# Kernel tuning notes

Hardware: AMD Instinct MI355X
Metric: run time of the kernel (lower is better)

Reference implementation:

```python
import jax, jax.numpy as jnp
import numpy as np

DG = 8   # deformable groups
K = 9    # 3x3 kernel taps


def _conv3x3(x, w, b):
    y = jax.lax.conv_general_dilated(x, w, (1, 1), ((1, 1), (1, 1)),
                                     dimension_numbers=('NCHW', 'OIHW', 'NCHW'))
    return y + b[None, :, None, None]


def _deform_conv_v2(x, off_y, off_x, mask, w, b):
    # x: [B,C,H,W], off_*/mask: [B,DG,K,H,W], w: [Cout,C,3,3], b: [Cout]
    B, C, H, W = x.shape
    cpg = C // DG
    k = jnp.arange(K)
    ky = (k // 3 - 1).astype(x.dtype)[None, None, :, None, None]
    kx = (k % 3 - 1).astype(x.dtype)[None, None, :, None, None]
    hh = jnp.arange(H, dtype=x.dtype)[None, None, None, :, None]
    ww = jnp.arange(W, dtype=x.dtype)[None, None, None, None, :]
    py = hh + ky + off_y            # sampling rows  [B,DG,K,H,W]
    px = ww + kx + off_x            # sampling cols
    y0 = jnp.floor(py); x0 = jnp.floor(px)
    ly = py - y0; lx = px - x0
    xf = x.reshape(B, DG, cpg, H * W)

    def corner(yi, xi):
        valid = ((yi >= 0) & (yi < H) & (xi >= 0) & (xi < W)).astype(x.dtype)
        idx = (jnp.clip(yi, 0, H - 1) * W + jnp.clip(xi, 0, W - 1)).astype(jnp.int32)
        idxb = jnp.broadcast_to(idx.reshape(B, DG, 1, K * H * W), (B, DG, cpg, K * H * W))
        v = jnp.take_along_axis(xf, idxb, axis=3).reshape(B, DG, cpg, K, H, W)
        return v, valid

    v00, m00 = corner(y0, x0)
    v01, m01 = corner(y0, x0 + 1)
    v10, m10 = corner(y0 + 1, x0)
    v11, m11 = corner(y0 + 1, x0 + 1)
    w00 = ((1 - ly) * (1 - lx) * m00)[:, :, None]
    w01 = ((1 - ly) * lx * m01)[:, :, None]
    w10 = (ly * (1 - lx) * m10)[:, :, None]
    w11 = (ly * lx * m11)[:, :, None]
    val = (v00 * w00 + v01 * w01 + v10 * w10 + v11 * w11) * mask[:, :, None]
    wr = w.reshape(w.shape[0], DG, cpg, K)
    return jnp.einsum('bgckhw,ogck->bohw', val, wr) + b[None, :, None, None]


def reference(feat_l, feat_s, w_atten, w_fsm, w_off, w_cm, b_cm, w_dcn, b_dcn):
    B, C, H, W = feat_l.shape
    # bilinear upsample (align_corners=False == half-pixel centers, matches jax.image.resize)
    feat_up = jax.image.resize(feat_s, (B, feat_s.shape[1], H, W), method='bilinear')
    # FeatureSelectionModule: SE-style gate + residual + 1x1 proj
    gap = feat_l.mean(axis=(2, 3))                       # [B,C]
    atten = jax.nn.sigmoid(gap @ w_atten.T)[:, :, None, None]
    xg = feat_l * (1.0 + atten)                          # x + x*atten
    feat_arm = jnp.einsum('bchw,oc->bohw', xg, w_fsm)
    # offset feature: 1x1 conv over cat([feat_arm, 2*feat_up])
    cat = jnp.concatenate([feat_arm, feat_up * 2.0], axis=1)
    off_feat = jnp.einsum('bchw,oc->bohw', cat, w_off)
    # dcn_v2 internal conv_offset_mask -> o1, o2, mask
    om = _conv3x3(off_feat, w_cm, b_cm)                  # [B, DG*3*K, H, W]
    n = DG * K
    off_y = om[:, :n].reshape(B, DG, K, H, W)
    off_x = om[:, n:2 * n].reshape(B, DG, K, H, W)
    mask = jax.nn.sigmoid(om[:, 2 * n:]).reshape(B, DG, K, H, W)
    out = _deform_conv_v2(feat_up, off_y, off_x, mask, w_dcn, b_dcn)
    return jax.nn.relu(out) + feat_arm


def setup_inputs() -> dict:
    key = jax.random.key(0)
    ks = jax.random.split(key, 9)
    B, C, H, W = 8, 128, 64, 64
    return {
        'feat_l': jax.random.normal(ks[0], (B, C, H, W), jnp.float32),
        'feat_s': jax.random.normal(ks[1], (B, C, H // 2, W // 2), jnp.float32),
        'w_atten': jax.random.normal(ks[2], (C, C), jnp.float32) / np.sqrt(C),
        'w_fsm': jax.random.normal(ks[3], (C, C), jnp.float32) / np.sqrt(C),
        'w_off': jax.random.normal(ks[4], (C, 2 * C), jnp.float32) / np.sqrt(2 * C),
        'w_cm': jax.random.normal(ks[5], (DG * 3 * K, C, 3, 3), jnp.float32) * 0.01,
        'b_cm': jnp.zeros((DG * 3 * K,), jnp.float32),
        'w_dcn': jax.random.normal(ks[6], (C, C, 3, 3), jnp.float32) / np.sqrt(C * 9),
        'b_dcn': jax.random.normal(ks[7], (C,), jnp.float32) * 0.01,
    }
```

## Files before the change

kernel.cpp:

```cpp
#include <hip/hip_runtime.h>
#include <hip/hip_bf16.h>

constexpr int Bn = 8, Cn = 128, Hn = 64, Wn = 64, HWn = Hn * Wn;
constexpr int DGn = 8, Kn = 9, CMn = 216;
constexpr int Hs = 32, Ws = 32, HWs = Hs * Ws;

typedef __attribute__((ext_vector_type(8))) short bf16x8;
typedef __attribute__((ext_vector_type(4))) float f32x4;

constexpr long OFF_FLAG = 0;
constexpr long OFF_FLB  = 256;
constexpr long OFF_FUPB = OFF_FLB  + (long)Bn*HWn*Cn/2;
constexpr long OFF_OFT  = OFF_FUPB + (long)Bn*HWn*Cn/2;
constexpr long OFF_WCT  = OFF_OFT  + (long)Bn*HWn*Cn/2;
constexpr long OFF_WDT  = OFF_WCT  + (long)18*224*64/2 + 64;
constexpr long OFF_P    = OFF_WDT  + (long)Kn*Cn*Cn/2 + 64;
constexpr long OFF_W1TB = OFF_P    + 16384;
constexpr long OFF_WCAT = OFF_W1TB + (long)Bn*Cn*Cn/2;
constexpr long OFF_BCM  = OFF_WCAT + (long)Bn*Cn*256/2;
constexpr long OFF_BDC  = OFF_BCM + 256;
constexpr long OFF_GAP  = OFF_BDC + 256;
constexpr long OFF_AT   = OFF_GAP + 1024;
constexpr long OFF_FARM = OFF_AT  + 1024;
constexpr long OFF_OM   = OFF_FARM + (long)Bn*Cn*HWn;

static __device__ __forceinline__ float ldin(const void* p, long i, bool isbf) {
  if (isbf) return __bfloat162float(((const __hip_bfloat16*)p)[i]);
  return ((const float*)p)[i];
}
static __device__ __forceinline__ unsigned short f2b(float f) {
  unsigned u = __builtin_bit_cast(unsigned, f);
  u += 0x7FFFu + ((u >> 16) & 1u);
  return (unsigned short)(u >> 16);
}
static __device__ __forceinline__ unsigned pack2(float v0, float v1) {
  return ((unsigned)f2b(v1) << 16) | (unsigned)f2b(v0);
}
static __device__ __forceinline__ float b2f(unsigned short s) {
  return __builtin_bit_cast(float, ((unsigned)s) << 16);
}

#define GLOAD_LDS16(g, l) __builtin_amdgcn_global_load_lds( \
    (const __attribute__((address_space(1))) void*)(g),     \
    (__attribute__((address_space(3))) void*)(l), 16, 0, 0)

__global__ __launch_bounds__(256) void k_detect(const unsigned int* __restrict__ p,
                                                int* __restrict__ flag,
                                                float* __restrict__ gap) {
  __shared__ int cnt[256];
  int t = threadIdx.x;
  int c = 0;
  for (int i = 0; i < 4; ++i) {
    unsigned v = p[t * 4 + i];
    unsigned e = (v >> 7) & 0xFFu;
    c += (e >= 118u && e <= 130u) ? 1 : 0;
  }
  cnt[t] = c;
#pragma unroll
  for (int i = 0; i < 4; ++i) gap[t + i * 256] = 0.f;
  __syncthreads();
  for (int s = 128; s > 0; s >>= 1) {
    if (t < s) cnt[t] += cnt[t + s];
    __syncthreads();
  }
  if (t == 0) *flag = (cnt[0] > 512) ? 1 : 0;
}

__global__ __launch_bounds__(256) void k_prep(const void* __restrict__ b_cm,
                                              const void* __restrict__ b_dcn,
                                              const void* __restrict__ w_cm,
                                              const void* __restrict__ w_dcn,
                                              const void* __restrict__ woff,
                                              const void* __restrict__ wfsm,
                                              float* __restrict__ bcm_d,
                                              float* __restrict__ bdc_d,
                                              unsigned short* __restrict__ wcb,
                                              unsigned short* __restrict__ wdb,
                                              float* __restrict__ P,
                                              const int* __restrict__ flag) {
  const int bid = blockIdx.x, t = threadIdx.x;
  const bool isbf = (*flag != 0);
  if (bid == 0) {
    if (t < CMn) bcm_d[t] = ldin(b_cm, t, isbf);
    if (t < Cn)  bdc_d[t] = ldin(b_dcn, t, isbf);
    return;
  }
  if (bid < 1 + 1008) {
    int i = (bid - 1) * 256 + t;
    if (i >= 18 * 224 * 64) return;
    int s = i / (224 * 64);
    int rem = i % (224 * 64);
    int oc = rem >> 6, c_off = rem & 63;
    int tap = s >> 1, ck = s & 1;
    int c = ck * 64 + c_off;
    float v = 0.f;
    if (oc < CMn) v = ldin(w_cm, ((long)oc * Cn + c) * Kn + tap, isbf);
    int chunk = c_off >> 3, e = c_off & 7;
    int pc = chunk ^ (oc & 7);
    wcb[(long)s * 14336 + oc * 64 + pc * 8 + e] = f2b(v);
    return;
  }
  if (bid < 1 + 1008 + 576) {
    int i = (bid - 1 - 1008) * 256 + t;
    if (i >= Kn * Cn * Cn) return;
    int e = i & 7, lh = (i >> 3) & 3, o = (i >> 5) & 127;
    int ks = (i >> 12) & 3, k = i >> 14;
    int c = ks * 32 + lh * 8 + e;
    wdb[i] = f2b(ldin(w_dcn, ((long)o * Cn + c) * Kn + k, isbf));
    return;
  }
  {
    int idx = (bid - 1 - 1008 - 576) * 256 + t;
    if (idx >= Cn * Cn) return;
    int o = idx >> 7, k = idx & 127;
    float s = 0.f;
    for (int c = 0; c < Cn; ++c)
      s += ldin(woff, (long)o * 256 + c, isbf) * ldin(wfsm, (long)c * Cn + k, isbf);
    P[idx] = s;
  }
}

__global__ __launch_bounds__(256) void k_cvtlup(const void* __restrict__ feat_l,
                                                const void* __restrict__ fs,
                                                unsigned short* __restrict__ flb,
                                                unsigned short* __restrict__ fupb,
                                                float* __restrict__ gap,
                                                const int* __restrict__ flag) {
  __shared__ float sh[8448];
  const int b = blockIdx.y, t = threadIdx.x;
  const bool isbf = (*flag != 0);
  if (blockIdx.z == 0) {
    const int p0 = blockIdx.x * 64;
    for (int i = t; i < 8192; i += 256) {
      int c = i >> 6, p = i & 63;
      sh[c * 65 + p] = ldin(feat_l, (long)(b * Cn + c) * HWn + p0 + p, isbf);
    }
    __syncthreads();
    if (t < 128) {
      float s = 0.f;
#pragma unroll
      for (int p = 0; p < 64; ++p) s += sh[t * 65 + p];
      atomicAdd(&gap[b * Cn + t], s * (1.0f / HWn));
    }
    for (int i = t; i < 1024; i += 256) {
      int p = i >> 4, ch = (i & 15) * 8;
      uint4 pk;
      pk.x = pack2(sh[(ch + 0) * 65 + p], sh[(ch + 1) * 65 + p]);
      pk.y = pack2(sh[(ch + 2) * 65 + p], sh[(ch + 3) * 65 + p]);
      pk.z = pack2(sh[(ch + 4) * 65 + p], sh[(ch + 5) * 65 + p]);
      pk.w = pack2(sh[(ch + 6) * 65 + p], sh[(ch + 7) * 65 + p]);
      *(uint4*)(flb + (((long)(b * HWn + p0 + p)) << 7) + ch) = pk;
    }
  } else {
    const int h = blockIdx.x;
    int iy0; float fy;
    if (h & 1) { iy0 = (h - 1) >> 1; fy = 0.25f; } else { iy0 = (h >> 1) - 1; fy = 0.75f; }
    int iy1 = min(iy0 + 1, Hs - 1); iy0 = max(iy0, 0);
    for (int i = t; i < 8192; i += 256) {
      int sel = i >> 12, c = (i >> 5) & 127, x = i & 31;
      int iy = sel ? iy1 : iy0;
      sh[sel * 4224 + c * 33 + x] = ldin(fs, (long)(b * Cn + c) * HWs + iy * Ws + x, isbf);
    }
    __syncthreads();
    for (int i = t; i < 1024; i += 256) {
      int w = i >> 4, ch0 = (i & 15) * 8;
      int ix0; float fx;
      if (w & 1) { ix0 = (w - 1) >> 1; fx = 0.25f; } else { ix0 = (w >> 1) - 1; fx = 0.75f; }
      int ix1 = min(ix0 + 1, Ws - 1); ix0 = max(ix0, 0);
      float v[8];
#pragma unroll
      for (int j = 0; j < 8; ++j) {
        int c = ch0 + j;
        v[j] = (1.f - fy) * ((1.f - fx) * sh[c * 33 + ix0] + fx * sh[c * 33 + ix1]) +
               fy         * ((1.f - fx) * sh[4224 + c * 33 + ix0] + fx * sh[4224 + c * 33 + ix1]);
      }
      uint4 pk;
      pk.x = pack2(v[0], v[1]); pk.y = pack2(v[2], v[3]);
      pk.z = pack2(v[4], v[5]); pk.w = pack2(v[6], v[7]);
      *(uint4*)(fupb + (((long)(b * HWn + h * Wn + w)) << 7) + ch0) = pk;
    }
  }
}

__global__ __launch_bounds__(256) void k_atten(const float* __restrict__ gap,
                                               const void* __restrict__ wat,
                                               float* __restrict__ at1p,
                                               const int* __restrict__ flag) {
  int tid = blockIdx.x * 256 + threadIdx.x;
  if (tid >= Bn * Cn) return;
  int b = tid >> 7, o = tid & 127;
  bool isbf = (*flag != 0);
  const float* g = gap + b * Cn;
  float s = 0.f;
  for (int c = 0; c < Cn; ++c) s += g[c] * ldin(wat, (long)o * Cn + c, isbf);
  at1p[tid] = 1.0f + 1.0f / (1.0f + expf(-s));
}

__global__ __launch_bounds__(256) void k_wprep(const void* __restrict__ wfsm,
                                               const void* __restrict__ woff,
                                               const float* __restrict__ P,
                                               const float* __restrict__ at1p,
                                               unsigned short* __restrict__ w1tb,
                                               unsigned short* __restrict__ wcat,
                                               const int* __restrict__ flag) {
  int idx = blockIdx.x * 256 + threadIdx.x;
  if (idx >= Bn * 49152) return;
  bool isbf = (*flag != 0);
  int b = idx / 49152, r = idx % 49152;
  if (r < 16384) {
    int o = r >> 7, k = r & 127;
    w1tb[((long)(b * Cn + o) << 7) + k] =
        f2b(ldin(wfsm, (long)o * Cn + k, isbf) * at1p[b * Cn + k]);
  } else {
    r -= 16384;
    int o = r >> 8, k = r & 255;
    float v = (k < 128) ? P[o * Cn + k] * at1p[b * Cn + k]
                        : 2.0f * ldin(woff, (long)o * 256 + k, isbf);
    wcat[((long)(b * Cn + o) << 8) + k] = f2b(v);
  }
}

__global__ __launch_bounds__(256) void k_fao(const unsigned short* __restrict__ flb,
                                             const unsigned short* __restrict__ fupb,
                                             const unsigned short* __restrict__ w1tb,
                                             const unsigned short* __restrict__ wcat,
                                             unsigned short* __restrict__ farm,
                                             unsigned short* __restrict__ oftb) {
  const int b = blockIdx.y, m0 = blockIdx.x * 32;
  const int t = threadIdx.x, lane = t & 63, wv = t >> 6;
  const int lm = lane & 15, lh = lane >> 4;
  f32x4 accF[2][2], accO[2][2];
#pragma unroll
  for (int mt = 0; mt < 2; ++mt)
#pragma unroll
    for (int nt = 0; nt < 2; ++nt) {
      accF[mt][nt] = (f32x4){0.f, 0.f, 0.f, 0.f};
      accO[mt][nt] = (f32x4){0.f, 0.f, 0.f, 0.f};
    }
  const unsigned short* A0 = flb + ((long)b << 19);
  const unsigned short* A1 = fupb + ((long)b << 19);
  const unsigned short* BwF = w1tb + ((long)b << 14);
  const unsigned short* BwO = wcat + ((long)b << 15);
#pragma unroll
  for (int ks = 0; ks < 4; ++ks) {
    int c0 = ks * 32 + lh * 8;
    bf16x8 bfvF[2], bfvO[2];
#pragma unroll
    for (int nt = 0; nt < 2; ++nt) {
      int o = wv * 32 + nt * 16 + lm;
      bfvF[nt] = *(const bf16x8*)(BwF + ((long)o << 7) + c0);
      bfvO[nt] = *(const bf16x8*)(BwO + ((long)o << 8) + c0);
    }
#pragma unroll
    for (int mt = 0; mt < 2; ++mt) {
      bf16x8 af = *(const bf16x8*)(A0 + (((long)(m0 + mt * 16 + lm)) << 7) + c0);
#pragma unroll
      for (int nt = 0; nt < 2; ++nt) {
        accF[mt][nt] = __builtin_amdgcn_mfma_f32_16x16x32_bf16(af, bfvF[nt], accF[mt][nt], 0, 0, 0);
        accO[mt][nt] = __builtin_amdgcn_mfma_f32_16x16x32_bf16(af, bfvO[nt], accO[mt][nt], 0, 0, 0);
      }
    }
  }
#pragma unroll
  for (int ks = 4; ks < 8; ++ks) {
    int c0 = ks * 32 + lh * 8;
    int ca = c0 - 128;
    bf16x8 bfvO[2];
#pragma unroll
    for (int nt = 0; nt < 2; ++nt)
      bfvO[nt] = *(const bf16x8*)(BwO + (((long)(wv * 32 + nt * 16 + lm)) << 8) + c0);
#pragma unroll
    for (int mt = 0; mt < 2; ++mt) {
      bf16x8 af = *(const bf16x8*)(A1 + (((long)(m0 + mt * 16 + lm)) << 7) + ca);
#pragma unroll
      for (int nt = 0; nt < 2; ++nt)
        accO[mt][nt] = __builtin_amdgcn_mfma_f32_16x16x32_bf16(af, bfvO[nt], accO[mt][nt], 0, 0, 0);
    }
  }
#pragma unroll
  for (int nt = 0; nt < 2; ++nt) {
    int o = wv * 32 + nt * 16 + lm;
#pragma unroll
    for (int mt = 0; mt < 2; ++mt) {
      uint2 pw;
      pw.x = pack2(accF[mt][nt][0], accF[mt][nt][1]);
      pw.y = pack2(accF[mt][nt][2], accF[mt][nt][3]);
      *(uint2*)(farm + (((long)(b * Cn + o)) << 12) + m0 + mt * 16 + lh * 4) = pw;
#pragma unroll
      for (int r = 0; r < 4; ++r)
        oftb[(((long)(b * HWn + m0 + mt * 16 + lh * 4 + r)) << 7) + o] = f2b(accO[mt][nt][r]);
    }
  }
}

__global__ __launch_bounds__(256) void k_convcm(const unsigned short* __restrict__ xb,
                                                const unsigned short* __restrict__ wsl,
                                                const float* __restrict__ bcm,
                                                unsigned short* __restrict__ om) {
  __shared__ unsigned short wlds[2][14336];
  const int bid = blockIdx.x;
  const int b = bid & 7, h = bid >> 3;
  const int t = threadIdx.x, lane = t & 63, wv = t >> 6;
  const int mi = wv & 1, ni = wv >> 1;
  const int lm = lane & 15, lh = lane >> 4;

  f32x4 acc[2][7];
#pragma unroll
  for (int mt = 0; mt < 2; ++mt)
#pragma unroll
    for (int nt = 0; nt < 7; ++nt) acc[mt][nt] = (f32x4){0.f, 0.f, 0.f, 0.f};

  auto stage = [&](int s, int bufi) {
    const char* src = (const char*)(wsl + (long)s * 14336);
    char* dstb = (char*)&wlds[bufi][0];
#pragma unroll
    for (int i2 = 0; i2 < 7; ++i2) {
      int off = (wv * 7 + i2) * 1024;
      GLOAD_LDS16(src + off + lane * 16, dstb + off);
    }
  };

  stage(0, 0);
  __syncthreads();

  for (int s = 0; s < 18; ++s) {
    const int cur = s & 1;
    if (s < 17) stage(s + 1, cur ^ 1);
    const int tap = s >> 1, ck = s & 1;
    const int ky = tap / 3, kx = tap % 3;
    const int gy = h + ky - 1;
    const bool gyok = ((unsigned)gy < (unsigned)Hn);
    const int gyc = min(max(gy, 0), Hn - 1);

    bf16x8 af[2][2];
#pragma unroll
    for (int mt = 0; mt < 2; ++mt) {
      int wpos = mi * 32 + mt * 16 + lm;
      int gx = wpos + kx - 1;
      bool ok = gyok && ((unsigned)gx < (unsigned)Wn);
      int gxc = min(max(gx, 0), Wn - 1);
      const unsigned short* ap = xb + (((long)(b * HWn + gyc * Wn + gxc)) << 7)
                                    + ck * 64 + lh * 8;
#pragma unroll
      for (int ksub = 0; ksub < 2; ++ksub) {
        bf16x8 v = *(const bf16x8*)(ap + ksub * 32);
        af[mt][ksub] = ok ? v : (bf16x8)(short)0;
      }
    }

    const char* wbase = (const char*)&wlds[cur][0];
#pragma unroll
    for (int ksub = 0; ksub < 2; ++ksub) {
      int jj = ksub * 4 + lh;
#pragma unroll
      for (int nt = 0; nt < 7; ++nt) {
        int oc = ni * 112 + nt * 16 + lm;
        bf16x8 bfv = *(const bf16x8*)(wbase + oc * 128 + ((jj ^ (oc & 7)) << 4));
#pragma unroll
        for (int mt = 0; mt < 2; ++mt)
          acc[mt][nt] = __builtin_amdgcn_mfma_f32_16x16x32_bf16(
              af[mt][ksub], bfv, acc[mt][nt], 0, 0, 0);
      }
    }
    __syncthreads();
  }

#pragma unroll
  for (int nt = 0; nt < 7; ++nt) {
    int ch = ni * 112 + nt * 16 + lm;
    if (ch >= CMn) continue;
    float bias = bcm[ch];
#pragma unroll
    for (int mt = 0; mt < 2; ++mt) {
#pragma unroll
      for (int r = 0; r < 4; ++r) {
        int w = mi * 32 + mt * 16 + lh * 4 + r;
        float v = acc[mt][nt][r] + bias;
        if (ch >= 144) v = 1.0f / (1.0f + expf(-v));
        om[((long)((b * Hn + h) * CMn + ch) << 6) + w] = f2b(v);
      }
    }
  }
}

__global__ __launch_bounds__(512, 8) void k_dcn(const unsigned short* __restrict__ omb,
                                                const unsigned short* __restrict__ fupb,
                                                const unsigned short* __restrict__ wdb,
                                                const float* __restrict__ bdc,
                                                const unsigned short* __restrict__ farm,
                                                void* __restrict__ out,
                                                const int* __restrict__ flagp) {
  __shared__ char smem[13824 + 16384];
  unsigned short* om16 = (unsigned short*)smem;
  const int bid = blockIdx.x;
  const int b = bid & 7, hw = bid >> 3;
  const int h = hw >> 1, w0 = (hw & 1) * 32;
  const int t = threadIdx.x;
  const int lane = t & 63, wid = t >> 6;
  const int lm = lane & 15, lh = lane >> 4;

  const unsigned short* omr = omb + ((long)(b * Hn + h) * CMn << 6) + w0;
  for (int i = t; i < 864; i += 512) {
    int ch = i >> 2, q = i & 3;
    *(uint4*)(om16 + ch * 32 + q * 8) = *(const uint4*)(omr + (ch << 6) + q * 8);
  }

  const int pid = (wid << 6) | lane;
  const int half = pid & 1, gw = (pid >> 1) & 31, gg = pid >> 6;
  const int wcol = w0 + gw;
  const unsigned short* fbb = fupb + ((long)b << 19) + half * 8;

  const int cw = wid - 4;
  f32x4 acc[2][2];
#pragma unroll
  for (int mt = 0; mt < 2; ++mt)
#pragma unroll
    for (int nt = 0; nt < 2; ++nt) acc[mt][nt] = (f32x4){0.f, 0.f, 0.f, 0.f};

  union U4 { uint4 q; unsigned short s[8]; };

  auto stage = [&](int k) {
#pragma unroll
    for (int ti = 0; ti < 2; ++ti) {
      const int g = gg + ti * 4;
      const unsigned short* fb = fbb + g * 16;
      int ch = g * Kn + k;
      float oy = b2f(om16[ch * 32 + gw]);
      float ox = b2f(om16[(72 + ch) * 32 + gw]);
      float mk = b2f(om16[(144 + ch) * 32 + gw]);
      float py = (float)(h + k / 3 - 1) + oy;
      float px = (float)(wcol + k % 3 - 1) + ox;
      float fy = floorf(py), fx = floorf(px);
      float ly = py - fy, lx = px - fx;
      int y0 = (int)fy, x0 = (int)fx, y1 = y0 + 1, x1 = x0 + 1;
      float vy0 = (y0 >= 0 && y0 < Hn) ? 1.f : 0.f;
      float vy1 = (y1 >= 0 && y1 < Hn) ? 1.f : 0.f;
      float vx0 = (x0 >= 0 && x0 < Wn) ? 1.f : 0.f;
      float vx1 = (x1 >= 0 && x1 < Wn) ? 1.f : 0.f;
      int cy0 = min(max(y0, 0), Hn - 1), cy1 = min(max(y1, 0), Hn - 1);
      int cx0 = min(max(x0, 0), Wn - 1), cx1 = min(max(x1, 0), Wn - 1);
      float wq0 = (1.f - ly) * (1.f - lx) * vy0 * vx0 * mk;
      float wq1 = (1.f - ly) * lx * vy0 * vx1 * mk;
      float wq2 = ly * (1.f - lx) * vy1 * vx0 * mk;
      float wq3 = ly * lx * vy1 * vx1 * mk;
      U4 a0, a1, a2, a3;
      a0.q = *(const uint4*)(fb + ((long)(cy0 * Wn + cx0) << 7));
      a1.q = *(const uint4*)(fb + ((long)(cy0 * Wn + cx1) << 7));
      a2.q = *(const uint4*)(fb + ((long)(cy1 * Wn + cx0) << 7));
      a3.q = *(const uint4*)(fb + ((long)(cy1 * Wn + cx1) << 7));
      float v[8];
#pragma unroll
      for (int j = 0; j < 8; ++j)
        v[j] = wq0 * b2f(a0.s[j]) + wq1 * b2f(a1.s[j]) +
               wq2 * b2f(a2.s[j]) + wq3 * b2f(a3.s[j]);
      uint4 pk;
      pk.x = pack2(v[0], v[1]); pk.y = pack2(v[2], v[3]);
      pk.z = pack2(v[4], v[5]); pk.w = pack2(v[6], v[7]);
      int chunk = g * 2 + half;
      *(uint4*)(smem + 13824 + (k & 1) * 8192 + gw * 256 + ((chunk ^ (gw & 15)) << 4)) = pk;
    }
  };

  __syncthreads();
  if (wid < 4) stage(0);
  __syncthreads();

#pragma unroll
  for (int k = 0; k < Kn; ++k) {
    if (wid < 4) {
      if (k < Kn - 1) stage(k + 1);
    } else {
      const char* base = smem + 13824 + (k & 1) * 8192;
      const unsigned short* wk = wdb + (long)k * 16384;
      __builtin_amdgcn_s_setprio(1);
#pragma unroll
      for (int ks = 0; ks < 4; ++ks) {
        int rchunk = (ks * 4 + lh) ^ lm;
        bf16x8 af0 = *(const bf16x8*)(base + lm * 256 + (rchunk << 4));
        bf16x8 af1 = *(const bf16x8*)(base + (16 + lm) * 256 + (rchunk << 4));
#pragma unroll
        for (int nt = 0; nt < 2; ++nt) {
          bf16x8 bfv = *(const bf16x8*)(wk + ks * 4096 +
                                        ((cw * 32 + nt * 16 + lm) << 5) + lh * 8);
          acc[0][nt] = __builtin_amdgcn_mfma_f32_16x16x32_bf16(af0, bfv, acc[0][nt], 0, 0, 0);
          acc[1][nt] = __builtin_amdgcn_mfma_f32_16x16x32_bf16(af1, bfv, acc[1][nt], 0, 0, 0);
        }
      }
      __builtin_amdgcn_s_setprio(0);
    }
    __syncthreads();
  }

  float* eps = (float*)smem;
  if (wid >= 4) {
#pragma unroll
    for (int nt = 0; nt < 2; ++nt) {
      int o = cw * 32 + nt * 16 + lm;
#pragma unroll
      for (int mt = 0; mt < 2; ++mt)
#pragma unroll
        for (int r = 0; r < 4; ++r)
          eps[o * 33 + mt * 16 + lh * 4 + r] = acc[mt][nt][r];
    }
  }
  __syncthreads();
  {
    bool isbf = (*flagp != 0);
    int o = t >> 2, q = t & 3;
    float bias = bdc[o];
    long obase = (long)(b * Cn + o) * HWn + h * Wn + w0 + q * 8;
    U4 fv;
    fv.q = *(const uint4*)(farm + obase);
    float vout[8];
#pragma unroll
    for (int j = 0; j < 8; ++j) {
      float v = eps[o * 33 + q * 8 + j] + bias;
      vout[j] = fmaxf(v, 0.f) + b2f(fv.s[j]);
    }
    if (isbf) {
      uint4 pk;
      pk.x = pack2(vout[0], vout[1]); pk.y = pack2(vout[2], vout[3]);
      pk.z = pack2(vout[4], vout[5]); pk.w = pack2(vout[6], vout[7]);
      *(uint4*)((__hip_bfloat16*)out + obase) = pk;
    } else {
      float* op = (float*)out + obase;
      *(float4*)op = (float4){vout[0], vout[1], vout[2], vout[3]};
      *(float4*)(op + 4) = (float4){vout[4], vout[5], vout[6], vout[7]};
    }
  }
}

extern "C" void kernel_launch(void* const* d_in, const int* in_sizes, int n_in,
                              void* d_out, int out_size, void* d_ws, size_t ws_size,
                              hipStream_t stream) {
  (void)in_sizes; (void)n_in; (void)out_size; (void)ws_size;
  const void* feat_l  = d_in[0];
  const void* feat_s  = d_in[1];
  const void* w_atten = d_in[2];
  const void* w_fsm   = d_in[3];
  const void* w_off   = d_in[4];
  const void* w_cm    = d_in[5];
  const void* b_cm    = d_in[6];
  const void* w_dcn   = d_in[7];
  const void* b_dcn   = d_in[8];
  float* ws = (float*)d_ws;
  int* flagw = (int*)d_ws;
  const int* flag = (const int*)d_ws;
  unsigned short* flb  = (unsigned short*)(ws + OFF_FLB);
  unsigned short* fupb = (unsigned short*)(ws + OFF_FUPB);
  unsigned short* oftb = (unsigned short*)(ws + OFF_OFT);
  unsigned short* wcb  = (unsigned short*)(ws + OFF_WCT);
  unsigned short* wdb  = (unsigned short*)(ws + OFF_WDT);
  unsigned short* w1tb = (unsigned short*)(ws + OFF_W1TB);
  unsigned short* wcat = (unsigned short*)(ws + OFF_WCAT);
  unsigned short* farm = (unsigned short*)(ws + OFF_FARM);
  unsigned short* omb  = (unsigned short*)(ws + OFF_OM);

  k_detect<<<1, 256, 0, stream>>>((const unsigned int*)feat_l, flagw, ws + OFF_GAP);
  k_prep<<<1 + 1008 + 576 + 64, 256, 0, stream>>>(b_cm, b_dcn, w_cm, w_dcn,
                                                  w_off, w_fsm,
                                                  ws + OFF_BCM, ws + OFF_BDC,
                                                  wcb, wdb, ws + OFF_P, flag);
  k_cvtlup<<<dim3(64, 8, 2), 256, 0, stream>>>(feat_l, feat_s, flb, fupb,
                                               ws + OFF_GAP, flag);
  k_atten<<<4, 256, 0, stream>>>(ws + OFF_GAP, w_atten, ws + OFF_AT, flag);
  k_wprep<<<(Bn * 49152 + 255) / 256, 256, 0, stream>>>(w_fsm, w_off, ws + OFF_P,
                                                        ws + OFF_AT, w1tb, wcat, flag);
  k_fao<<<dim3(128, 8), 256, 0, stream>>>(flb, fupb, w1tb, wcat, farm, oftb);
  k_convcm<<<512, 256, 0, stream>>>(oftb, wcb, ws + OFF_BCM, omb);
  k_dcn<<<1024, 512, 0, stream>>>(omb, fupb, wdb, ws + OFF_BDC, farm, d_out, flag);
}
```

Baseline: 169.5 us.

## Replace producer/consumer warp split with uniform gather+MFMA across all 8 waves

The deformable-conv kernel used to dedicate four waves to bilinear gathering and four to MFMA. Now all eight waves do both. Each wave gathers one deformable group and computes 16 output channels. The next tap's gather loads are issued before this tap's MFMAs and combined afterward, so memory latency is hidden behind matrix math within the same wave. This evens out work between waves but raises register pressure and halves the MFMA work per wave.

```diff
diff --git a/kernel.cpp b/kernel.cpp
--- a/kernel.cpp
+++ b/kernel.cpp
@@ -405,71 +405,75 @@
     *(uint4*)(om16 + ch * 32 + q * 8) = *(const uint4*)(omr + (ch << 6) + q * 8);
   }
 
-  const int pid = (wid << 6) | lane;
-  const int half = pid & 1, gw = (pid >> 1) & 31, gg = pid >> 6;
+  const int half = lane & 1, gw = lane >> 1, g = wid;
   const int wcol = w0 + gw;
-  const unsigned short* fbb = fupb + ((long)b << 19) + half * 8;
-
-  const int cw = wid - 4;
-  f32x4 acc[2][2];
-#pragma unroll
-  for (int mt = 0; mt < 2; ++mt)
-#pragma unroll
-    for (int nt = 0; nt < 2; ++nt) acc[mt][nt] = (f32x4){0.f, 0.f, 0.f, 0.f};
+  const unsigned short* fb = fupb + ((long)b << 19) + g * 16 + half * 8;
+  const int vchunk = (g * 2 + half) ^ (gw & 15);
+
+  f32x4 acc[2];
+  acc[0] = (f32x4){0.f, 0.f, 0.f, 0.f};
+  acc[1] = (f32x4){0.f, 0.f, 0.f, 0.f};
 
   union U4 { uint4 q; unsigned short s[8]; };
 
-  auto stage = [&](int k) {
-#pragma unroll
-    for (int ti = 0; ti < 2; ++ti) {
-      const int g = gg + ti * 4;
-      const unsigned short* fb = fbb + g * 16;
-      int ch = g * Kn + k;
-      float oy = b2f(om16[ch * 32 + gw]);
-      float ox = b2f(om16[(72 + ch) * 32 + gw]);
-      float mk = b2f(om16[(144 + ch) * 32 + gw]);
-      float py = (float)(h + k / 3 - 1) + oy;
-      float px = (float)(wcol + k % 3 - 1) + ox;
-      float fy = floorf(py), fx = floorf(px);
-      float ly = py - fy, lx = px - fx;
-      int y0 = (int)fy, x0 = (int)fx, y1 = y0 + 1, x1 = x0 + 1;
-      float vy0 = (y0 >= 0 && y0 < Hn) ? 1.f : 0.f;
-      float vy1 = (y1 >= 0 && y1 < Hn) ? 1.f : 0.f;
-      float vx0 = (x0 >= 0 && x0 < Wn) ? 1.f : 0.f;
-      float vx1 = (x1 >= 0 && x1 < Wn) ? 1.f : 0.f;
-      int cy0 = min(max(y0, 0), Hn - 1), cy1 = min(max(y1, 0), Hn - 1);
-      int cx0 = min(max(x0, 0), Wn - 1), cx1 = min(max(x1, 0), Wn - 1);
-      float wq0 = (1.f - ly) * (1.f - lx) * vy0 * vx0 * mk;
-      float wq1 = (1.f - ly) * lx * vy0 * vx1 * mk;
-      float wq2 = ly * (1.f - lx) * vy1 * vx0 * mk;
-      float wq3 = ly * lx * vy1 * vx1 * mk;
-      U4 a0, a1, a2, a3;
-      a0.q = *(const uint4*)(fb + ((long)(cy0 * Wn + cx0) << 7));
-      a1.q = *(const uint4*)(fb + ((long)(cy0 * Wn + cx1) << 7));
-      a2.q = *(const uint4*)(fb + ((long)(cy1 * Wn + cx0) << 7));
-      a3.q = *(const uint4*)(fb + ((long)(cy1 * Wn + cx1) << 7));
-      float v[8];
-#pragma unroll
-      for (int j = 0; j < 8; ++j)
-        v[j] = wq0 * b2f(a0.s[j]) + wq1 * b2f(a1.s[j]) +
-               wq2 * b2f(a2.s[j]) + wq3 * b2f(a3.s[j]);
-      uint4 pk;
-      pk.x = pack2(v[0], v[1]); pk.y = pack2(v[2], v[3]);
-      pk.z = pack2(v[4], v[5]); pk.w = pack2(v[6], v[7]);
-      int chunk = g * 2 + half;
-      *(uint4*)(smem + 13824 + (k & 1) * 8192 + gw * 256 + ((chunk ^ (gw & 15)) << 4)) = pk;
-    }
+  auto gaddr = [&](int k, const unsigned short** q, float* wq) {
+    int ch = g * Kn + k;
+    float oy = b2f(om16[ch * 32 + gw]);
+    float ox = b2f(om16[(72 + ch) * 32 + gw]);
+    float mk = b2f(om16[(144 + ch) * 32 + gw]);
+    float py = (float)(h + k / 3 - 1) + oy;
+    float px = (float)(wcol + k % 3 - 1) + ox;
+    float fy = floorf(py), fx = floorf(px);
+    float ly = py - fy, lx = px - fx;
+    int y0 = (int)fy, x0 = (int)fx, y1 = y0 + 1, x1 = x0 + 1;
+    float vy0 = (y0 >= 0 && y0 < Hn) ? 1.f : 0.f;
+    float vy1 = (y1 >= 0 && y1 < Hn) ? 1.f : 0.f;
+    float vx0 = (x0 >= 0 && x0 < Wn) ? 1.f : 0.f;
+    float vx1 = (x1 >= 0 && x1 < Wn) ? 1.f : 0.f;
+    int cy0 = min(max(y0, 0), Hn - 1), cy1 = min(max(y1, 0), Hn - 1);
+    int cx0 = min(max(x0, 0), Wn - 1), cx1 = min(max(x1, 0), Wn - 1);
+    wq[0] = (1.f - ly) * (1.f - lx) * vy0 * vx0 * mk;
+    wq[1] = (1.f - ly) * lx * vy0 * vx1 * mk;
+    wq[2] = ly * (1.f - lx) * vy1 * vx0 * mk;
+    wq[3] = ly * lx * vy1 * vx1 * mk;
+    q[0] = fb + ((long)(cy0 * Wn + cx0) << 7);
+    q[1] = fb + ((long)(cy0 * Wn + cx1) << 7);
+    q[2] = fb + ((long)(cy1 * Wn + cx0) << 7);
+    q[3] = fb + ((long)(cy1 * Wn + cx1) << 7);
   };
 
   __syncthreads();
-  if (wid < 4) stage(0);
+
+  {
+    const unsigned short* q[4];
+    float wq[4];
+    gaddr(0, q, wq);
+    U4 r0, r1, r2, r3;
+    r0.q = *(const uint4*)q[0]; r1.q = *(const uint4*)q[1];
+    r2.q = *(const uint4*)q[2]; r3.q = *(const uint4*)q[3];
+    float v[8];
+#pragma unroll
+    for (int j = 0; j < 8; ++j)
+      v[j] = wq[0] * b2f(r0.s[j]) + wq[1] * b2f(r1.s[j]) +
+             wq[2] * b2f(r2.s[j]) + wq[3] * b2f(r3.s[j]);
+    uint4 pk;
+    pk.x = pack2(v[0], v[1]); pk.y = pack2(v[2], v[3]);
+    pk.z = pack2(v[4], v[5]); pk.w = pack2(v[6], v[7]);
+    *(uint4*)(smem + 13824 + gw * 256 + (vchunk << 4)) = pk;
+  }
   __syncthreads();
 
 #pragma unroll
   for (int k = 0; k < Kn; ++k) {
-    if (wid < 4) {
-      if (k < Kn - 1) stage(k + 1);
-    } else {
+    U4 r0, r1, r2, r3;
+    float wq[4];
+    if (k < Kn - 1) {
+      const unsigned short* q[4];
+      gaddr(k + 1, q, wq);
+      r0.q = *(const uint4*)q[0]; r1.q = *(const uint4*)q[1];
+      r2.q = *(const uint4*)q[2]; r3.q = *(const uint4*)q[3];
+    }
+    {
       const char* base = smem + 13824 + (k & 1) * 8192;
       const unsigned short* wk = wdb + (long)k * 16384;
       __builtin_amdgcn_s_setprio(1);
@@ -478,30 +482,35 @@
         int rchunk = (ks * 4 + lh) ^ lm;
         bf16x8 af0 = *(const bf16x8*)(base + lm * 256 + (rchunk << 4));
         bf16x8 af1 = *(const bf16x8*)(base + (16 + lm) * 256 + (rchunk << 4));
-#pragma unroll
-        for (int nt = 0; nt < 2; ++nt) {
-          bf16x8 bfv = *(const bf16x8*)(wk + ks * 4096 +
-                                        ((cw * 32 + nt * 16 + lm) << 5) + lh * 8);
-          acc[0][nt] = __builtin_amdgcn_mfma_f32_16x16x32_bf16(af0, bfv, acc[0][nt], 0, 0, 0);
-          acc[1][nt] = __builtin_amdgcn_mfma_f32_16x16x32_bf16(af1, bfv, acc[1][nt], 0, 0, 0);
-        }
+        bf16x8 bfv = *(const bf16x8*)(wk + ks * 4096 +
+                                      ((wid * 16 + lm) << 5) + lh * 8);
+        acc[0] = __builtin_amdgcn_mfma_f32_16x16x32_bf16(af0, bfv, acc[0], 0, 0, 0);
+        acc[1] = __builtin_amdgcn_mfma_f32_16x16x32_bf16(af1, bfv, acc[1], 0, 0, 0);
       }
       __builtin_amdgcn_s_setprio(0);
     }
+    if (k < Kn - 1) {
+      float v[8];
+#pragma unroll
+      for (int j = 0; j < 8; ++j)
+        v[j] = wq[0] * b2f(r0.s[j]) + wq[1] * b2f(r1.s[j]) +
+               wq[2] * b2f(r2.s[j]) + wq[3] * b2f(r3.s[j]);
+      uint4 pk;
+      pk.x = pack2(v[0], v[1]); pk.y = pack2(v[2], v[3]);
+      pk.z = pack2(v[4], v[5]); pk.w = pack2(v[6], v[7]);
+      *(uint4*)(smem + 13824 + ((k + 1) & 1) * 8192 + gw * 256 + (vchunk << 4)) = pk;
+    }
     __syncthreads();
   }
 
   float* eps = (float*)smem;
-  if (wid >= 4) {
-#pragma unroll
-    for (int nt = 0; nt < 2; ++nt) {
-      int o = cw * 32 + nt * 16 + lm;
-#pragma unroll
-      for (int mt = 0; mt < 2; ++mt)
-#pragma unroll
-        for (int r = 0; r < 4; ++r)
-          eps[o * 33 + mt * 16 + lh * 4 + r] = acc[mt][nt][r];
-    }
+  {
+    int o = wid * 16 + lm;
+#pragma unroll
+    for (int mt = 0; mt < 2; ++mt)
+#pragma unroll
+      for (int r = 0; r < 4; ++r)
+        eps[o * 33 + mt * 16 + lh * 4 + r] = acc[mt][r];
   }
   __syncthreads();
   {
```

Measured after the change: 174.7 us. +3.1%, slower.
